# Optimization experiments

Measured on AMD Instinct MI355X. Metric: run time of the kernel, lower is better.

The kernel has to match this reference:

```python
import jax, jax.numpy as jnp
import numpy as np

ALPHA = 16
M_FACTORS = [8, 16, 8]
N_FACTORS = [8, 16, 8]


def setup_inputs() -> dict:
    key = jax.random.key(0)
    ks = jax.random.split(key, 9)
    B, S, D = 8, 2048, 1024
    r = 8
    x = jax.random.normal(ks[0], (B, S, D), dtype=jnp.float32)
    W = jax.random.normal(ks[1], (D, D), dtype=jnp.float32) * 0.02
    b = jax.random.normal(ks[2], (D,), dtype=jnp.float32) * 0.02
    # m-cores: (r_prev, m_i, r_next), first rank = 1
    core0 = jax.random.normal(ks[3], (1, 8, r), dtype=jnp.float32) * 0.1
    core1 = jax.random.normal(ks[4], (r, 16, r), dtype=jnp.float32) * 0.1
    core2 = jax.random.normal(ks[5], (r, 8, r), dtype=jnp.float32) * 0.1
    # n-cores: (r_prev, n_i, r_next), last rank = 1
    core3 = jax.random.normal(ks[6], (r, 8, r), dtype=jnp.float32) * 0.1
    core4 = jax.random.normal(ks[7], (r, 16, r), dtype=jnp.float32) * 0.1
    core5 = jax.random.normal(ks[8], (r, 8, 1), dtype=jnp.float32) * 0.1
    return {"x": x, "W": W, "b": b, "core0": core0, "core1": core1,
            "core2": core2, "core3": core3, "core4": core4, "core5": core5}


def tensorized_multiplication(x, m_cores, n_cores, m_factors):
    B, S, _ = x.shape
    # [B, 1, S, m_k, ..., m_1] : input dim split into m_factors, reversed
    tt = x.reshape((B, S) + tuple(m_factors[::-1]))[:, None]
    for core in m_cores:
        # contract trailing m-factor and current rank, new rank at axis 1
        tt = jnp.einsum('br...m,rmp->bp...', tt, core)
    for core in n_cores:
        # expand n-factor at the end, carry rank at axis 1
        tt = jnp.einsum('br...,rnp->bp...n', tt, core)
    # tt: [B, 1, S, n_1, ..., n_k] -> [B, S, prod(n_factors)]
    return tt.reshape(B, S, -1)


def reference(x, W, b, core0, core1, core2, core3, core4, core5):
    z = tensorized_multiplication(x, [core0, core1, core2],
                                  [core3, core4, core5], M_FACTORS)
    base = jnp.einsum('bsd,od->bso', x, W) + b  # nn.Linear: x @ W.T + b
    return base + z * ALPHA
```

## Files before the change

### kernel.cpp

```cpp
#include <hip/hip_runtime.h>
#include <hip/hip_bf16.h>


#define D_DIM 1024
#define BS_ROWS 16384
#define ALPHA_F 16.0f
#define BM 128
#define BN 128

using bf16   = __bf16;
using bf16x8 = __attribute__((ext_vector_type(8))) __bf16;
using bf16x4 = __attribute__((ext_vector_type(4))) __bf16;
using f32x4  = __attribute__((ext_vector_type(4))) float;

#define GPTR(p) (const __attribute__((address_space(1))) void*)(p)
#define SPTR(p) (__attribute__((address_space(3))) void*)(p)

__global__ __launch_bounds__(256) void make_mn_kernel(
    const float* __restrict__ c0, const float* __restrict__ c1,
    const float* __restrict__ c2, const float* __restrict__ c3,
    const float* __restrict__ c4, const float* __restrict__ c5,
    float* __restrict__ Mws, float* __restrict__ NTws)
{
    __shared__ float sh[128 * 9];
    const int tid = threadIdx.x;

    if (blockIdx.x < 32) {
        for (int e = tid; e < 1024; e += 256) {
            int p2 = e & 7, i2i1 = e >> 3;
            int i1 = i2i1 & 7, i2 = i2i1 >> 3;
            float s = 0.f;
            for (int p1 = 0; p1 < 8; ++p1)
                s += c0[i1 * 8 + p1] * c1[p1 * 128 + i2 * 8 + p2];
            sh[i2i1 * 9 + p2] = s;
        }
        __syncthreads();
        int e = blockIdx.x * 256 + tid;
        int p3 = e & 7, d = e >> 3;
        int i1 = d & 7, i2 = (d >> 3) & 15, i3 = d >> 7;
        float s = 0.f;
        for (int p2 = 0; p2 < 8; ++p2)
            s += sh[(i2 * 8 + i1) * 9 + p2] * c2[p2 * 64 + i3 * 8 + p3];
        Mws[e] = s;
    } else {
        for (int e = tid; e < 1024; e += 256) {
            int p4 = e & 7, nn = e >> 3;
            int n2 = nn >> 3, n3 = nn & 7;
            float s = 0.f;
            for (int p5 = 0; p5 < 8; ++p5)
                s += c4[p4 * 128 + n2 * 8 + p5] * c5[p5 * 8 + n3];
            sh[nn * 9 + p4] = s;
        }
        __syncthreads();
        int e = (blockIdx.x - 32) * 256 + tid;
        int r3 = e & 7, o = e >> 3;
        int n1 = o >> 7, nn = o & 127;
        float s = 0.f;
        for (int p4 = 0; p4 < 8; ++p4)
            s += c3[r3 * 64 + n1 * 8 + p4] * sh[nn * 9 + p4];
        NTws[o * 8 + r3] = s;
    }
}

__global__ __launch_bounds__(256) void weff_cast_kernel(
    const float* __restrict__ X, const float* __restrict__ W,
    const float* __restrict__ Mws, const float* __restrict__ NTws,
    bf16* __restrict__ Weff, bf16* __restrict__ Xb)
{
    const int tid = threadIdx.x;
    if (blockIdx.x >= 512) {
        size_t i = ((size_t)(blockIdx.x - 512) * 256 + tid) * 8;
        f32x4 a = *(const f32x4*)&X[i];
        f32x4 b = *(const f32x4*)&X[i + 4];
        bf16x8 v;
        v[0] = (bf16)a[0]; v[1] = (bf16)a[1]; v[2] = (bf16)a[2]; v[3] = (bf16)a[3];
        v[4] = (bf16)b[0]; v[5] = (bf16)b[1]; v[6] = (bf16)b[2]; v[7] = (bf16)b[3];
        *(bf16x8*)&Xb[i] = v;
        return;
    }
    int e  = blockIdx.x * 256 + tid;
    int o  = e >> 7;
    int d0 = (e & 127) * 8;
    f32x4 nt0 = *(const f32x4*)&NTws[o * 8];
    f32x4 nt1 = *(const f32x4*)&NTws[o * 8 + 4];
    f32x4 w0 = *(const f32x4*)&W[(size_t)o * D_DIM + d0];
    f32x4 w1 = *(const f32x4*)&W[(size_t)o * D_DIM + d0 + 4];
    bf16x8 res;
    for (int k = 0; k < 8; ++k) {
        f32x4 m0 = *(const f32x4*)&Mws[(d0 + k) * 8];
        f32x4 m1 = *(const f32x4*)&Mws[(d0 + k) * 8 + 4];
        float acc = m0[0]*nt0[0] + m0[1]*nt0[1] + m0[2]*nt0[2] + m0[3]*nt0[3]
                  + m1[0]*nt1[0] + m1[1]*nt1[1] + m1[2]*nt1[2] + m1[3]*nt1[3];
        float w = (k < 4) ? w0[k] : w1[k - 4];
        res[k] = (bf16)(w + ALPHA_F * acc);
    }
    *(bf16x8*)&Weff[(size_t)o * D_DIM + d0] = res;
}

#define TBM 256
#define TBN 256
#define TBK 64
#define ABYT 32768
#define BUF6 65536
#define NT6  (D_DIM / TBK)

__global__ __launch_bounds__(512, 2) void gemm_pipe6_kernel(
    const bf16* __restrict__ Xb,
    const bf16* __restrict__ Weff,
    const float* __restrict__ bias,
    float* __restrict__ Out)
{
    extern __shared__ __attribute__((aligned(16))) char smem[];

    const int tid  = threadIdx.x;
    const int wave = tid >> 6, lane = tid & 63;

    const int bid   = blockIdx.x;
    const int slot  = (bid & 7) * 32 + (bid >> 3);
    const int mtile = slot >> 2;
    const int ntile = slot & 3;

    const int wr = wave >> 2, wc = wave & 3;
    const int l15 = lane & 15, quad = lane >> 4;
    const int rsw = l15 & 7;

    const int urow   = wave * 8 + (lane >> 3);
    const int gchunk = (lane & 7) ^ (lane >> 3);
    const bf16* aB = Xb   + (size_t)(mtile * TBM) * D_DIM + gchunk * 8;
    const bf16* bB = Weff + (size_t)(ntile * TBN) * D_DIM + gchunk * 8;
    const int lco = wave * 1024 + lane * 16;

    auto STAGE_UNIT = [&](int bo, int t, int u) {
        const bf16* src = (u < 2)
            ? aB + (size_t)(u * 128 + urow) * D_DIM + t * TBK
            : bB + (size_t)((u - 2) * 128 + urow) * D_DIM + t * TBK;
        char* dst = smem + bo + (u < 2 ? 0 : ABYT) + (u & 1) * 16384 + lco;
#pragma unroll
        for (int j = 0; j < 2; ++j)
            __builtin_amdgcn_global_load_lds(GPTR(src + (size_t)j * 64 * D_DIM),
                                             SPTR(dst + j * 8192), 16, 0, 0);
    };

    f32x4 acc[8][4];
#pragma unroll
    for (int i = 0; i < 8; ++i)
#pragma unroll
        for (int j = 0; j < 4; ++j)
#pragma unroll
            for (int r = 0; r < 4; ++r) acc[i][j][r] = 0.f;

    STAGE_UNIT(0, 0, 2); STAGE_UNIT(0, 0, 3);
    STAGE_UNIT(0, 0, 0); STAGE_UNIT(0, 0, 1);
    asm volatile("s_waitcnt vmcnt(0)" ::: "memory");
    __builtin_amdgcn_s_barrier();
    __builtin_amdgcn_sched_barrier(0);

    for (int t = 0; t < NT6; ++t) {
        const int bo = (t & 1) * BUF6;
        const int bn = ((t + 1) & 1) * BUF6;
        const bool more = (t + 1 < NT6);
        const char* Ab = smem + bo;
        const char* Bb = smem + bo + ABYT;

        bf16x8 bfr[4][2];
#pragma unroll
        for (int p = 0; p < 4; ++p) {
            if (p == 0 && more) { STAGE_UNIT(bn, t + 1, 2); STAGE_UNIT(bn, t + 1, 3); }
            if (p == 1 && more) { STAGE_UNIT(bn, t + 1, 0); STAGE_UNIT(bn, t + 1, 1); }

            if (p == 0) {
#pragma unroll
                for (int j = 0; j < 4; ++j)
#pragma unroll
                    for (int kk = 0; kk < 2; ++kk)
                        bfr[j][kk] = *(const bf16x8*)(Bb
                            + (wc * 64 + j * 16 + l15) * 128
                            + ((kk * 4 + quad) ^ rsw) * 16);
            }
            bf16x8 af[2][2];
#pragma unroll
            for (int ii = 0; ii < 2; ++ii)
#pragma unroll
                for (int kk = 0; kk < 2; ++kk)
                    af[ii][kk] = *(const bf16x8*)(Ab
                        + (wr * 128 + (2 * p + ii) * 16 + l15) * 128
                        + ((kk * 4 + quad) ^ rsw) * 16);

            __builtin_amdgcn_s_barrier();
            asm volatile("s_waitcnt lgkmcnt(0)" ::: "memory");
            __builtin_amdgcn_s_setprio(1);
#pragma unroll
            for (int kk = 0; kk < 2; ++kk)
#pragma unroll
                for (int ii = 0; ii < 2; ++ii)
#pragma unroll
                    for (int j = 0; j < 4; ++j)
                        acc[2 * p + ii][j] = __builtin_amdgcn_mfma_f32_16x16x32_bf16(
                            af[ii][kk], bfr[j][kk], acc[2 * p + ii][j], 0, 0, 0);
            __builtin_amdgcn_s_setprio(0);
            if (p < 3) __builtin_amdgcn_s_barrier();
        }

        if (more) {
            asm volatile("s_waitcnt vmcnt(0)" ::: "memory");
            __builtin_amdgcn_s_barrier();
            __builtin_amdgcn_sched_barrier(0);
        }
    }

    float bj[4];
#pragma unroll
    for (int j = 0; j < 4; ++j)
        bj[j] = bias[ntile * TBN + wc * 64 + j * 16 + l15];
#pragma unroll
    for (int i = 0; i < 8; ++i) {
        int row0 = mtile * TBM + wr * 128 + i * 16 + quad * 4;
#pragma unroll
        for (int r = 0; r < 4; ++r) {
            float* orow = Out + (size_t)(row0 + r) * D_DIM + ntile * TBN + wc * 64 + l15;
#pragma unroll
            for (int j = 0; j < 4; ++j)
                orow[j * 16] = acc[i][j][r] + bj[j];
        }
    }
}

__global__ __launch_bounds__(256) void gemm_bb_kernel(
    const bf16* __restrict__ Xb,
    const bf16* __restrict__ Weff,
    const float* __restrict__ bias,
    float* __restrict__ Out)
{
    __shared__ __align__(16) bf16 As[BM][64];
    __shared__ __align__(16) bf16 Bs[BN][64];

    const int tid  = threadIdx.x;
    const int wave = tid >> 6, lane = tid & 63;
    const int mtile = blockIdx.x, ntile = blockIdx.y;
    const int wr = wave >> 1, wc = wave & 1;
    const int l15 = lane & 15, quad = lane >> 4;

    const int srow = wave * 32 + (lane >> 3);
    const int gchunk = (lane & 7) ^ (lane >> 3);
    const bf16* asrc = Xb   + (size_t)(mtile * BM + srow) * D_DIM + gchunk * 8;
    const bf16* bsrc = Weff + (size_t)(ntile * BN + srow) * D_DIM + gchunk * 8;
    char* abase = (char*)&As[0][0] + wave * 4096;
    char* bbase = (char*)&Bs[0][0] + wave * 4096;

    const int rsw = l15 & 7;

    f32x4 acc[4][4];
    for (int i = 0; i < 4; ++i)
        for (int j = 0; j < 4; ++j)
            for (int r = 0; r < 4; ++r) acc[i][j][r] = 0.f;

    for (int kt = 0; kt < D_DIM / 64; ++kt) {
        const int ko = kt * 64;
        for (int j = 0; j < 4; ++j) {
            __builtin_amdgcn_global_load_lds(GPTR(asrc + (size_t)j * 8 * D_DIM + ko),
                                             SPTR(abase + j * 1024), 16, 0, 0);
            __builtin_amdgcn_global_load_lds(GPTR(bsrc + (size_t)j * 8 * D_DIM + ko),
                                             SPTR(bbase + j * 1024), 16, 0, 0);
        }
        __syncthreads();
        for (int kk = 0; kk < 2; ++kk) {
            const int lc = kk * 4 + quad;
            const int sc = (lc ^ rsw) * 8;
            bf16x8 af[4], bfr[4];
            for (int i = 0; i < 4; ++i)
                af[i] = *(const bf16x8*)&As[wr * 64 + i * 16 + l15][sc];
            for (int j = 0; j < 4; ++j)
                bfr[j] = *(const bf16x8*)&Bs[wc * 64 + j * 16 + l15][sc];
            for (int i = 0; i < 4; ++i)
                for (int j = 0; j < 4; ++j)
                    acc[i][j] = __builtin_amdgcn_mfma_f32_16x16x32_bf16(
                        af[i], bfr[j], acc[i][j], 0, 0, 0);
        }
        __syncthreads();
    }

    float bj[4];
    for (int j = 0; j < 4; ++j)
        bj[j] = bias[ntile * BN + wc * 64 + j * 16 + l15];
    for (int i = 0; i < 4; ++i) {
        int row0 = mtile * BM + wr * 64 + i * 16 + quad * 4;
        for (int r = 0; r < 4; ++r) {
            float* orow = Out + (size_t)(row0 + r) * D_DIM + ntile * BN + wc * 64 + l15;
            for (int j = 0; j < 4; ++j)
                orow[j * 16] = acc[i][j][r] + bj[j];
        }
    }
}

__global__ __launch_bounds__(256) void gemm_bias_kernel(
    const float* __restrict__ X,
    const bf16* __restrict__ Weff,
    const float* __restrict__ bias,
    float* __restrict__ Out)
{
    __shared__ __align__(16) bf16 As[BM][32];
    __shared__ __align__(16) bf16 Bs[BN][32];

    const int tid  = threadIdx.x;
    const int wave = tid >> 6, lane = tid & 63;
    const int mtile = blockIdx.x, ntile = blockIdx.y;
    const int wr = wave >> 1, wc = wave & 1;
    const int l15 = lane & 15, quad = lane >> 4;

    const int ar = tid >> 1, ah = tid & 1;
    const float* xsrc = X + (size_t)(mtile * BM + ar) * D_DIM + ah * 16;
    bf16* adst = &As[ar][ah * 16];

    const bf16* bsrc0 = Weff + (size_t)(ntile * BN + wave * 32 + (lane >> 2)) * D_DIM
                        + (lane & 3) * 8;
    const bf16* bsrc1 = bsrc0 + 16 * D_DIM;
    char* bbase = (char*)&Bs[0][0];
    void* bdst0 = bbase + wave * 2048;
    void* bdst1 = bbase + wave * 2048 + 1024;

    f32x4 acc[4][4];
    for (int i = 0; i < 4; ++i)
        for (int j = 0; j < 4; ++j)
            for (int r = 0; r < 4; ++r) acc[i][j][r] = 0.f;

    for (int kt = 0; kt < D_DIM / 32; ++kt) {
        __builtin_amdgcn_global_load_lds(GPTR(bsrc0 + kt * 32), SPTR(bdst0), 16, 0, 0);
        __builtin_amdgcn_global_load_lds(GPTR(bsrc1 + kt * 32), SPTR(bdst1), 16, 0, 0);

        const f32x4* xp = (const f32x4*)(xsrc + kt * 32);
        f32x4 f0 = xp[0], f1 = xp[1], f2 = xp[2], f3 = xp[3];
        bf16x8 p0, p1;
        p0[0] = (bf16)f0[0]; p0[1] = (bf16)f0[1]; p0[2] = (bf16)f0[2]; p0[3] = (bf16)f0[3];
        p0[4] = (bf16)f1[0]; p0[5] = (bf16)f1[1]; p0[6] = (bf16)f1[2]; p0[7] = (bf16)f1[3];
        p1[0] = (bf16)f2[0]; p1[1] = (bf16)f2[1]; p1[2] = (bf16)f2[2]; p1[3] = (bf16)f2[3];
        p1[4] = (bf16)f3[0]; p1[5] = (bf16)f3[1]; p1[6] = (bf16)f3[2]; p1[7] = (bf16)f3[3];
        *(bf16x8*)adst = p0;
        *(bf16x8*)(adst + 8) = p1;

        __syncthreads();

        bf16x8 af[4], bfr[4];
        for (int i = 0; i < 4; ++i)
            af[i] = *(const bf16x8*)&As[wr * 64 + i * 16 + l15][quad * 8];
        for (int j = 0; j < 4; ++j)
            bfr[j] = *(const bf16x8*)&Bs[wc * 64 + j * 16 + l15][quad * 8];
        for (int i = 0; i < 4; ++i)
            for (int j = 0; j < 4; ++j)
                acc[i][j] = __builtin_amdgcn_mfma_f32_16x16x32_bf16(
                    af[i], bfr[j], acc[i][j], 0, 0, 0);

        __syncthreads();
    }

    float bj[4];
    for (int j = 0; j < 4; ++j)
        bj[j] = bias[ntile * BN + wc * 64 + j * 16 + l15];
    for (int i = 0; i < 4; ++i) {
        int row0 = mtile * BM + wr * 64 + i * 16 + quad * 4;
        for (int r = 0; r < 4; ++r) {
            float* orow = Out + (size_t)(row0 + r) * D_DIM + ntile * BN + wc * 64 + l15;
            for (int j = 0; j < 4; ++j)
                orow[j * 16] = acc[i][j][r] + bj[j];
        }
    }
}

__global__ __launch_bounds__(256) void build_weff_fused_kernel(
    const float* __restrict__ W,
    const float* __restrict__ c0, const float* __restrict__ c1,
    const float* __restrict__ c2, const float* __restrict__ c3,
    const float* __restrict__ c4, const float* __restrict__ c5,
    bf16* __restrict__ Weff)
{
    __shared__ float t2[1024];
    __shared__ float Msh[8192];
    const int tid = threadIdx.x;
    const int o = blockIdx.x;

    for (int e = tid; e < 1024; e += 256) {
        int p2 = e & 7, i2i1 = e >> 3;
        int i1 = i2i1 & 7, i2 = i2i1 >> 3;
        float s = 0.f;
        for (int p1 = 0; p1 < 8; ++p1)
            s += c0[i1 * 8 + p1] * c1[p1 * 128 + i2 * 8 + p2];
        t2[e] = s;
    }
    __syncthreads();
    for (int e = tid; e < 8192; e += 256) {
        int p3 = e & 7, d = e >> 3;
        int i1 = d & 7, i2 = (d >> 3) & 15, i3 = d >> 7;
        float s = 0.f;
        for (int p2 = 0; p2 < 8; ++p2)
            s += t2[(i2 * 8 + i1) * 8 + p2] * c2[p2 * 64 + i3 * 8 + p3];
        Msh[e] = s;
    }
    int n1 = o >> 7, nn = o & 127, n2 = nn >> 3, n3 = nn & 7;
    float v[8];
    for (int p4 = 0; p4 < 8; ++p4) {
        float s = 0.f;
        for (int p5 = 0; p5 < 8; ++p5)
            s += c4[p4 * 128 + n2 * 8 + p5] * c5[p5 * 8 + n3];
        v[p4] = s;
    }
    float ncol[8];
    for (int r3 = 0; r3 < 8; ++r3) {
        float s = 0.f;
        for (int p4 = 0; p4 < 8; ++p4)
            s += c3[r3 * 64 + n1 * 8 + p4] * v[p4];
        ncol[r3] = s;
    }
    __syncthreads();

    int d0 = tid * 4;
    f32x4 w = *(const f32x4*)&W[o * D_DIM + d0];
    bf16x4 res;
    for (int k = 0; k < 4; ++k) {
        float acc = 0.f;
        for (int r = 0; r < 8; ++r)
            acc += Msh[(d0 + k) * 8 + r] * ncol[r];
        res[k] = (bf16)(w[k] + ALPHA_F * acc);
    }
    *(bf16x4*)&Weff[o * D_DIM + d0] = res;
}

extern "C" void kernel_launch(void* const* d_in, const int* in_sizes, int n_in,
                              void* d_out, int out_size, void* d_ws, size_t ws_size,
                              hipStream_t stream) {
    const float* x  = (const float*)d_in[0];
    const float* W  = (const float*)d_in[1];
    const float* b  = (const float*)d_in[2];
    const float* c0 = (const float*)d_in[3];
    const float* c1 = (const float*)d_in[4];
    const float* c2 = (const float*)d_in[5];
    const float* c3 = (const float*)d_in[6];
    const float* c4 = (const float*)d_in[7];
    const float* c5 = (const float*)d_in[8];
    float* out = (float*)d_out;

    char* ws = (char*)d_ws;
    bf16*  Weff = (bf16*)ws;
    float* Mws  = (float*)(ws + 2u * 1024u * 1024u);
    float* NTws = Mws + 8192;
    bf16*  Xb   = (bf16*)(ws + 4u * 1024u * 1024u);
    const size_t need = 4u * 1024u * 1024u + (size_t)BS_ROWS * D_DIM * 2u;

    static int smem_ok = -1;
    if (smem_ok < 0) {
        hipError_t e = hipFuncSetAttribute((const void*)gemm_pipe6_kernel,
                                           hipFuncAttributeMaxDynamicSharedMemorySize,
                                           2 * BUF6);
        smem_ok = (e == hipSuccess) ? 1 : 0;
    }

    if (ws_size >= need) {
        make_mn_kernel<<<64, 256, 0, stream>>>(c0, c1, c2, c3, c4, c5, Mws, NTws);
        weff_cast_kernel<<<512 + 8192, 256, 0, stream>>>(x, W, Mws, NTws, Weff, Xb);
        if (smem_ok) {
            gemm_pipe6_kernel<<<dim3(256), 512, 2 * BUF6, stream>>>(Xb, Weff, b, out);
        } else {
            dim3 grid(BS_ROWS / BM, D_DIM / BN);
            gemm_bb_kernel<<<grid, 256, 0, stream>>>(Xb, Weff, b, out);
        }
    } else {
        build_weff_fused_kernel<<<D_DIM, 256, 0, stream>>>(W, c0, c1, c2, c3, c4, c5, Weff);
        dim3 grid(BS_ROWS / BM, D_DIM / BN);
        gemm_bias_kernel<<<grid, 256, 0, stream>>>(x, Weff, b, out);
    }
}
```

Before: 165.5 us.

## Restructure GEMM pipeline with partial vmcnt waits and all-at-once prefetch

Rewrites the main loop of the bf16 GEMM so that all eight global-to-LDS loads for the next K tile are issued at the start of each iteration. Fine-grained vmcnt waits then let each phase wait only for the rows it needs, and the last tile is peeled into its own epilogue. This aims to shorten the end-of-iteration full vmcnt(0) stall and overlap more of the loads with MFMA work. It adds extra barriers and more ordering-sensitive wait counts, which could cause stalls or correctness risks if the counts do not match the issue order.

After: 165.6 us. Within noise of the previous version (+0.1%).

```diff
diff --git a/kernel.cpp b/kernel.cpp
--- a/kernel.cpp
+++ b/kernel.cpp
@@ -101,10 +101,10 @@
 #define TBN 256
 #define TBK 64
 #define ABYT 32768
-#define BUF6 65536
-#define NT6  (D_DIM / TBK)
-
-__global__ __launch_bounds__(512, 2) void gemm_pipe6_kernel(
+#define BUF7 65536
+#define NT7  (D_DIM / TBK)
+
+__global__ __launch_bounds__(512, 2) void gemm_pipe7_kernel(
     const bf16* __restrict__ Xb,
     const bf16* __restrict__ Weff,
     const float* __restrict__ bias,
@@ -130,16 +130,19 @@
     const bf16* bB = Weff + (size_t)(ntile * TBN) * D_DIM + gchunk * 8;
     const int lco = wave * 1024 + lane * 16;
 
-    auto STAGE_UNIT = [&](int bo, int t, int u) {
+    auto ISSUE = [&](int bo, int t, int u, int j) {
         const bf16* src = (u < 2)
-            ? aB + (size_t)(u * 128 + urow) * D_DIM + t * TBK
-            : bB + (size_t)((u - 2) * 128 + urow) * D_DIM + t * TBK;
-        char* dst = smem + bo + (u < 2 ? 0 : ABYT) + (u & 1) * 16384 + lco;
-#pragma unroll
-        for (int j = 0; j < 2; ++j)
-            __builtin_amdgcn_global_load_lds(GPTR(src + (size_t)j * 64 * D_DIM),
-                                             SPTR(dst + j * 8192), 16, 0, 0);
+            ? aB + (size_t)(u * 128 + j * 64 + urow) * D_DIM + t * TBK
+            : bB + (size_t)((u - 2) * 128 + j * 64 + urow) * D_DIM + t * TBK;
+        char* dst = smem + bo + (u < 2 ? 0 : ABYT) + (u & 1) * 16384 + j * 8192 + lco;
+        __builtin_amdgcn_global_load_lds(GPTR(src), SPTR(dst), 16, 0, 0);
     };
+    auto STAGE_ALL = [&](int bo, int t) {
+        ISSUE(bo, t, 2, 0); ISSUE(bo, t, 2, 1);
+        ISSUE(bo, t, 3, 0); ISSUE(bo, t, 3, 1);
+        ISSUE(bo, t, 0, 0); ISSUE(bo, t, 1, 0);
+        ISSUE(bo, t, 0, 1); ISSUE(bo, t, 1, 1);
+    };
 
     f32x4 acc[8][4];
 #pragma unroll
@@ -149,62 +152,92 @@
 #pragma unroll
             for (int r = 0; r < 4; ++r) acc[i][j][r] = 0.f;
 
-    STAGE_UNIT(0, 0, 2); STAGE_UNIT(0, 0, 3);
-    STAGE_UNIT(0, 0, 0); STAGE_UNIT(0, 0, 1);
-    asm volatile("s_waitcnt vmcnt(0)" ::: "memory");
+    auto RD_B = [&](const char* Bb, bf16x8 bfr[4][2]) {
+#pragma unroll
+        for (int j = 0; j < 4; ++j)
+#pragma unroll
+            for (int kk = 0; kk < 2; ++kk)
+                bfr[j][kk] = *(const bf16x8*)(Bb + (wc * 64 + j * 16 + l15) * 128
+                                               + ((kk * 4 + quad) ^ rsw) * 16);
+    };
+    auto RD_A = [&](const char* Ab, int p, bf16x8 af[2][2]) {
+#pragma unroll
+        for (int ii = 0; ii < 2; ++ii)
+#pragma unroll
+            for (int kk = 0; kk < 2; ++kk)
+                af[ii][kk] = *(const bf16x8*)(Ab + (wr * 128 + (2 * p + ii) * 16 + l15) * 128
+                                               + ((kk * 4 + quad) ^ rsw) * 16);
+    };
+    auto FMA = [&](int p, bf16x8 af[2][2], bf16x8 bfr[4][2]) {
+        __builtin_amdgcn_s_setprio(1);
+#pragma unroll
+        for (int kk = 0; kk < 2; ++kk)
+#pragma unroll
+            for (int ii = 0; ii < 2; ++ii)
+#pragma unroll
+                for (int j = 0; j < 4; ++j)
+                    acc[2 * p + ii][j] = __builtin_amdgcn_mfma_f32_16x16x32_bf16(
+                        af[ii][kk], bfr[j][kk], acc[2 * p + ii][j], 0, 0, 0);
+        __builtin_amdgcn_s_setprio(0);
+    };
+
+    STAGE_ALL(0, 0);
+    asm volatile("s_waitcnt vmcnt(2)" ::: "memory");
     __builtin_amdgcn_s_barrier();
     __builtin_amdgcn_sched_barrier(0);
 
-    for (int t = 0; t < NT6; ++t) {
-        const int bo = (t & 1) * BUF6;
-        const int bn = ((t + 1) & 1) * BUF6;
-        const bool more = (t + 1 < NT6);
-        const char* Ab = smem + bo;
-        const char* Bb = smem + bo + ABYT;
-
-        bf16x8 bfr[4][2];
-#pragma unroll
-        for (int p = 0; p < 4; ++p) {
-            if (p == 0 && more) { STAGE_UNIT(bn, t + 1, 2); STAGE_UNIT(bn, t + 1, 3); }
-            if (p == 1 && more) { STAGE_UNIT(bn, t + 1, 0); STAGE_UNIT(bn, t + 1, 1); }
-
-            if (p == 0) {
-#pragma unroll
-                for (int j = 0; j < 4; ++j)
-#pragma unroll
-                    for (int kk = 0; kk < 2; ++kk)
-                        bfr[j][kk] = *(const bf16x8*)(Bb
-                            + (wc * 64 + j * 16 + l15) * 128
-                            + ((kk * 4 + quad) ^ rsw) * 16);
-            }
-            bf16x8 af[2][2];
-#pragma unroll
-            for (int ii = 0; ii < 2; ++ii)
-#pragma unroll
-                for (int kk = 0; kk < 2; ++kk)
-                    af[ii][kk] = *(const bf16x8*)(Ab
-                        + (wr * 128 + (2 * p + ii) * 16 + l15) * 128
-                        + ((kk * 4 + quad) ^ rsw) * 16);
-
-            __builtin_amdgcn_s_barrier();
+    for (int t = 0; t < NT7 - 1; ++t) {
+        const char* Ab = smem + (t & 1) * BUF7;
+        const char* Bb = Ab + ABYT;
+        const int bn = ((t + 1) & 1) * BUF7;
+        bf16x8 bfr[4][2], af[2][2];
+
+        RD_B(Bb, bfr); RD_A(Ab, 0, af);
+        STAGE_ALL(bn, t + 1);
+        __builtin_amdgcn_s_barrier();
+        asm volatile("s_waitcnt lgkmcnt(0)" ::: "memory");
+        __builtin_amdgcn_sched_barrier(0);
+        FMA(0, af, bfr);
+        __builtin_amdgcn_s_barrier();
+        RD_A(Ab, 1, af);
+        asm volatile("s_waitcnt vmcnt(8)" ::: "memory");
+        __builtin_amdgcn_s_barrier();
+        asm volatile("s_waitcnt lgkmcnt(0)" ::: "memory");
+        __builtin_amdgcn_sched_barrier(0);
+        FMA(1, af, bfr);
+        __builtin_amdgcn_s_barrier();
+        RD_A(Ab, 2, af);
+        __builtin_amdgcn_s_barrier();
+        asm volatile("s_waitcnt lgkmcnt(0)" ::: "memory");
+        __builtin_amdgcn_sched_barrier(0);
+        FMA(2, af, bfr);
+        __builtin_amdgcn_s_barrier();
+        RD_A(Ab, 3, af);
+        asm volatile("s_waitcnt vmcnt(2)" ::: "memory");
+        __builtin_amdgcn_s_barrier();
+        asm volatile("s_waitcnt lgkmcnt(0)" ::: "memory");
+        __builtin_amdgcn_sched_barrier(0);
+        FMA(3, af, bfr);
+        __builtin_amdgcn_s_barrier();
+    }
+
+    {
+        const char* Ab = smem + ((NT7 - 1) & 1) * BUF7;
+        const char* Bb = Ab + ABYT;
+        bf16x8 bfr[4][2], af[2][2];
+        RD_B(Bb, bfr); RD_A(Ab, 0, af);
+        asm volatile("s_waitcnt vmcnt(0)" ::: "memory");
+        __builtin_amdgcn_s_barrier();
+        asm volatile("s_waitcnt lgkmcnt(0)" ::: "memory");
+        __builtin_amdgcn_sched_barrier(0);
+        FMA(0, af, bfr);
+        __builtin_amdgcn_s_barrier();
+#pragma unroll
+        for (int p = 1; p < 4; ++p) {
+            RD_A(Ab, p, af);
             asm volatile("s_waitcnt lgkmcnt(0)" ::: "memory");
-            __builtin_amdgcn_s_setprio(1);
-#pragma unroll
-            for (int kk = 0; kk < 2; ++kk)
-#pragma unroll
-                for (int ii = 0; ii < 2; ++ii)
-#pragma unroll
-                    for (int j = 0; j < 4; ++j)
-                        acc[2 * p + ii][j] = __builtin_amdgcn_mfma_f32_16x16x32_bf16(
-                            af[ii][kk], bfr[j][kk], acc[2 * p + ii][j], 0, 0, 0);
-            __builtin_amdgcn_s_setprio(0);
-            if (p < 3) __builtin_amdgcn_s_barrier();
-        }
-
-        if (more) {
-            asm volatile("s_waitcnt vmcnt(0)" ::: "memory");
-            __builtin_amdgcn_s_barrier();
             __builtin_amdgcn_sched_barrier(0);
+            FMA(p, af, bfr);
         }
     }
 
@@ -446,9 +479,9 @@
 
     static int smem_ok = -1;
     if (smem_ok < 0) {
-        hipError_t e = hipFuncSetAttribute((const void*)gemm_pipe6_kernel,
+        hipError_t e = hipFuncSetAttribute((const void*)gemm_pipe7_kernel,
                                            hipFuncAttributeMaxDynamicSharedMemorySize,
-                                           2 * BUF6);
+                                           2 * BUF7);
         smem_ok = (e == hipSuccess) ? 1 : 0;
     }
 
@@ -456,7 +489,7 @@
         make_mn_kernel<<<64, 256, 0, stream>>>(c0, c1, c2, c3, c4, c5, Mws, NTws);
         weff_cast_kernel<<<512 + 8192, 256, 0, stream>>>(x, W, Mws, NTws, Weff, Xb);
         if (smem_ok) {
-            gemm_pipe6_kernel<<<dim3(256), 512, 2 * BUF6, stream>>>(Xb, Weff, b, out);
+            gemm_pipe7_kernel<<<dim3(256), 512, 2 * BUF7, stream>>>(Xb, Weff, b, out);
         } else {
             dim3 grid(BS_ROWS / BM, D_DIM / BN);
             gemm_bb_kernel<<<grid, 256, 0, stream>>>(Xb, Weff, b, out);
```
